# Performance work log

Hardware: AMD Instinct MI355X
Metric: run time of the kernel (lower is better)

The kernel has to match this reference:

```python
import jax, jax.numpy as jnp
import numpy as np

NOUN_VOCAB = 50000
FUNC_VOCAB = 10000
CTX_VOCAB = 50000
EMBED = 100
BATCH = 8192


def setup_inputs() -> dict:
    key = jax.random.key(0)
    k1, k2, k3, k4, k5, k6 = jax.random.split(key, 6)
    return {
        "X_argument": jax.random.randint(k1, (BATCH,), 0, NOUN_VOCAB, dtype=jnp.int32),
        "X_functor": jax.random.randint(k2, (BATCH,), 0, FUNC_VOCAB, dtype=jnp.int32),
        "X_context": jax.random.randint(k3, (BATCH,), 0, CTX_VOCAB, dtype=jnp.int32),
        # learned parameters
        "noun_matrix": jax.random.normal(k4, (NOUN_VOCAB, EMBED), dtype=jnp.float32),
        "functor_table": jax.random.normal(k5, (FUNC_VOCAB, EMBED * EMBED), dtype=jnp.float32),
        "context_table": jax.random.normal(k6, (CTX_VOCAB, EMBED), dtype=jnp.float32),
    }


def reference(X_argument, X_functor, X_context, noun_matrix, functor_table, context_table):
    arg_vecs = noun_matrix[X_argument]                       # [B, E]
    func_mats = functor_table[X_functor].reshape(-1, EMBED, EMBED)  # [B, E, E]
    ctx_vecs = context_table[X_context]                      # [B, E]
    # batched matvec (func matrix @ arg vector) then dot with context vector
    funcarg = jnp.einsum('bij,bj->bi', func_mats, arg_vecs)  # [B, E]
    return jnp.sum(funcarg * ctx_vecs, axis=1)               # [B]
```

## Files before the change

### kernel.cpp

```cpp
#include <hip/hip_runtime.h>

#define EMBED 100
#define MATSZ (EMBED * EMBED)
#define NVEC4 (MATSZ / 4)
#define BLOCK 256
#define ITERS 10

__global__ __launch_bounds__(BLOCK) void msg_kernel(
    const int* __restrict__ Xa,
    const int* __restrict__ Xf,
    const int* __restrict__ Xc,
    const float* __restrict__ noun_matrix,
    const float* __restrict__ functor_table,
    const float* __restrict__ context_table,
    float* __restrict__ out)
{
    const int b   = blockIdx.x;
    const int tid = threadIdx.x;

    __shared__ float4 s_arg4[EMBED / 4];
    __shared__ float  s_ctx[EMBED];
    __shared__ float  s_part[BLOCK / 64];

    const int ia  = Xa[b];
    const int ifn = Xf[b];
    const int ic  = Xc[b];

    if (tid < EMBED / 4) {
        s_arg4[tid] = ((const float4*)(noun_matrix + (size_t)ia * EMBED))[tid];
    }
    if (tid < EMBED) {
        s_ctx[tid] = context_table[(size_t)ic * EMBED + tid];
    }
    __syncthreads();

    const float4* __restrict__ M4 =
        (const float4*)(functor_table + (size_t)ifn * MATSZ);

    float4 mv[ITERS];
    #pragma unroll
    for (int k = 0; k < ITERS; ++k) {
        int v  = tid + k * BLOCK;
        int vc = v < NVEC4 ? v : (NVEC4 - 1);
        mv[k] = M4[vc];
    }

    float acc = 0.0f;
    #pragma unroll
    for (int k = 0; k < ITERS; ++k) {
        int v  = tid + k * BLOCK;
        int vc = v < NVEC4 ? v : (NVEC4 - 1);
        int f  = vc * 4;
        int i  = f / EMBED;
        int j  = f - i * EMBED;
        float4 a = s_arg4[j >> 2];
        float4 m = mv[k];
        float dot4 = m.x * a.x + m.y * a.y + m.z * a.z + m.w * a.w;
        float c = (v < NVEC4) ? s_ctx[i] : 0.0f;
        acc = fmaf(c, dot4, acc);
    }

    #pragma unroll
    for (int off = 32; off > 0; off >>= 1)
        acc += __shfl_down(acc, off, 64);

    const int wave = tid >> 6;
    const int lane = tid & 63;
    if (lane == 0) s_part[wave] = acc;
    __syncthreads();

    if (tid == 0) {
        float r = 0.0f;
        #pragma unroll
        for (int w = 0; w < BLOCK / 64; ++w) r += s_part[w];
        out[b] = r;
    }
}

extern "C" void kernel_launch(void* const* d_in, const int* in_sizes, int n_in,
                              void* d_out, int out_size, void* d_ws, size_t ws_size,
                              hipStream_t stream) {
    const int*   Xa   = (const int*)d_in[0];
    const int*   Xf   = (const int*)d_in[1];
    const int*   Xc   = (const int*)d_in[2];
    const float* noun = (const float*)d_in[3];
    const float* func = (const float*)d_in[4];
    const float* ctxt = (const float*)d_in[5];
    float*       out  = (float*)d_out;

    const int B = in_sizes[0];
    msg_kernel<<<B, BLOCK, 0, stream>>>(Xa, Xf, Xc, noun, func, ctxt, out);
}
```

Before: 509.6 us.

## Group batch rows by functor index to load each functor matrix once

Adds a workspace-based bucketing pass: a zero kernel and an atomic scatter kernel group batch indices by functor id (up to 8 per functor), plus a leftover list for any overflow. The main kernel then launches one block per functor vocabulary entry, loads that 40KB matrix once into registers and evaluates every batch row that uses it. This is meant to cut redundant reads of the functor table, since the 8192 rows draw from only 10000 functors and duplicates repeat the same matrix load. In exchange it adds three extra launches, atomics and per-row block syncs, and it launches 10000 blocks, most of which load nothing or exit early.

```diff
diff --git a/kernel.cpp b/kernel.cpp
--- a/kernel.cpp
+++ b/kernel.cpp
@@ -5,38 +5,58 @@
 #define NVEC4 (MATSZ / 4)
 #define BLOCK 256
 #define ITERS 10
+#define FUNC_VOCAB 10000
+#define K_CAP 8
+#define LEFT_BLOCKS 16
 
-__global__ __launch_bounds__(BLOCK) void msg_kernel(
+#define WS_COUNTS   0
+#define WS_LC       FUNC_VOCAB
+#define WS_BUCKET   10016
+#define WS_LEFT     (10016 + FUNC_VOCAB * K_CAP)
+
+__global__ __launch_bounds__(BLOCK) void zero_ws_kernel(int* __restrict__ w) {
+    int t = blockIdx.x * BLOCK + threadIdx.x;
+    if (t <= FUNC_VOCAB) w[t] = 0;
+}
+
+__global__ __launch_bounds__(BLOCK) void scatter_kernel(
+    const int* __restrict__ Xf, int* __restrict__ ws, int B)
+{
+    int t = blockIdx.x * BLOCK + threadIdx.x;
+    if (t >= B) return;
+    int f = Xf[t];
+    int slot = atomicAdd(&ws[WS_COUNTS + f], 1);
+    if (slot < K_CAP) {
+        ws[WS_BUCKET + f * K_CAP + slot] = t;
+    } else {
+        int s = atomicAdd(&ws[WS_LC], 1);
+        ws[WS_LEFT + s] = t;
+    }
+}
+
+__global__ __launch_bounds__(BLOCK) void pass2_kernel(
     const int* __restrict__ Xa,
-    const int* __restrict__ Xf,
     const int* __restrict__ Xc,
     const float* __restrict__ noun_matrix,
     const float* __restrict__ functor_table,
     const float* __restrict__ context_table,
-    float* __restrict__ out)
+    float* __restrict__ out,
+    const int* __restrict__ ws)
 {
-    const int b   = blockIdx.x;
+    const int f   = blockIdx.x;
     const int tid = threadIdx.x;
 
-    __shared__ float4 s_arg4[EMBED / 4];
-    __shared__ float  s_ctx[EMBED];
+    int c = ws[WS_COUNTS + f];
+    if (c <= 0) return;
+    if (c > K_CAP) c = K_CAP;
+
+    __shared__ float4 s_arg4[K_CAP][EMBED / 4];
+    __shared__ float  s_ctx [K_CAP][EMBED];
     __shared__ float  s_part[BLOCK / 64];
-
-    const int ia  = Xa[b];
-    const int ifn = Xf[b];
-    const int ic  = Xc[b];
-
-    if (tid < EMBED / 4) {
-        s_arg4[tid] = ((const float4*)(noun_matrix + (size_t)ia * EMBED))[tid];
-    }
-    if (tid < EMBED) {
-        s_ctx[tid] = context_table[(size_t)ic * EMBED + tid];
-    }
-    __syncthreads();
+    __shared__ int    s_b   [K_CAP];
 
     const float4* __restrict__ M4 =
-        (const float4*)(functor_table + (size_t)ifn * MATSZ);
-
+        (const float4*)(functor_table + (size_t)f * MATSZ);
     float4 mv[ITERS];
     #pragma unroll
     for (int k = 0; k < ITERS; ++k) {
@@ -45,35 +65,93 @@
         mv[k] = M4[vc];
     }
 
-    float acc = 0.0f;
-    #pragma unroll
-    for (int k = 0; k < ITERS; ++k) {
-        int v  = tid + k * BLOCK;
-        int vc = v < NVEC4 ? v : (NVEC4 - 1);
-        int f  = vc * 4;
-        int i  = f / EMBED;
-        int j  = f - i * EMBED;
-        float4 a = s_arg4[j >> 2];
-        float4 m = mv[k];
-        float dot4 = m.x * a.x + m.y * a.y + m.z * a.z + m.w * a.w;
-        float c = (v < NVEC4) ? s_ctx[i] : 0.0f;
-        acc = fmaf(c, dot4, acc);
+    const int p = tid >> 5;
+    const int r = tid & 31;
+    if (p < c) {
+        int b = ws[WS_BUCKET + f * K_CAP + p];
+        if (r == 0) s_b[p] = b;
+        if (r < EMBED / 4) {
+            s_arg4[p][r] = ((const float4*)(noun_matrix  + (size_t)Xa[b] * EMBED))[r];
+            ((float4*)s_ctx[p])[r] = ((const float4*)(context_table + (size_t)Xc[b] * EMBED))[r];
+        }
     }
-
-    #pragma unroll
-    for (int off = 32; off > 0; off >>= 1)
-        acc += __shfl_down(acc, off, 64);
-
-    const int wave = tid >> 6;
-    const int lane = tid & 63;
-    if (lane == 0) s_part[wave] = acc;
     __syncthreads();
 
-    if (tid == 0) {
-        float r = 0.0f;
+    for (int p2 = 0; p2 < c; ++p2) {
+        float acc = 0.0f;
         #pragma unroll
-        for (int w = 0; w < BLOCK / 64; ++w) r += s_part[w];
-        out[b] = r;
+        for (int k = 0; k < ITERS; ++k) {
+            int v  = tid + k * BLOCK;
+            int vc = v < NVEC4 ? v : (NVEC4 - 1);
+            int fi = vc * 4;
+            int i  = fi / EMBED;
+            int j  = fi - i * EMBED;
+            float4 a = s_arg4[p2][j >> 2];
+            float4 m = mv[k];
+            float d4 = m.x * a.x + m.y * a.y + m.z * a.z + m.w * a.w;
+            float cc = (v < NVEC4) ? s_ctx[p2][i] : 0.0f;
+            acc = fmaf(cc, d4, acc);
+        }
+        #pragma unroll
+        for (int off = 32; off > 0; off >>= 1)
+            acc += __shfl_down(acc, off, 64);
+        if ((tid & 63) == 0) s_part[tid >> 6] = acc;
+        __syncthreads();
+        if (tid == 0)
+            out[s_b[p2]] = s_part[0] + s_part[1] + s_part[2] + s_part[3];
+        __syncthreads();
+    }
+}
+
+__global__ __launch_bounds__(BLOCK) void leftover_kernel(
+    const int* __restrict__ Xa,
+    const int* __restrict__ Xf,
+    const int* __restrict__ Xc,
+    const float* __restrict__ noun_matrix,
+    const float* __restrict__ functor_table,
+    const float* __restrict__ context_table,
+    float* __restrict__ out,
+    const int* __restrict__ ws)
+{
+    const int tid = threadIdx.x;
+    const int n   = ws[WS_LC];
+
+    __shared__ float4 s_arg4[EMBED / 4];
+    __shared__ float  s_ctx[EMBED];
+    __shared__ float  s_part[BLOCK / 64];
+
+    for (int idx = blockIdx.x; idx < n; idx += LEFT_BLOCKS) {
+        int b = ws[WS_LEFT + idx];
+        if (tid < EMBED / 4) {
+            s_arg4[tid] = ((const float4*)(noun_matrix + (size_t)Xa[b] * EMBED))[tid];
+            ((float4*)s_ctx)[tid] = ((const float4*)(context_table + (size_t)Xc[b] * EMBED))[tid];
+        }
+        __syncthreads();
+
+        const float4* __restrict__ M4 =
+            (const float4*)(functor_table + (size_t)Xf[b] * MATSZ);
+        float acc = 0.0f;
+        #pragma unroll
+        for (int k = 0; k < ITERS; ++k) {
+            int v  = tid + k * BLOCK;
+            int vc = v < NVEC4 ? v : (NVEC4 - 1);
+            int fi = vc * 4;
+            int i  = fi / EMBED;
+            int j  = fi - i * EMBED;
+            float4 a = s_arg4[j >> 2];
+            float4 m = M4[vc];
+            float d4 = m.x * a.x + m.y * a.y + m.z * a.z + m.w * a.w;
+            float cc = (v < NVEC4) ? s_ctx[i] : 0.0f;
+            acc = fmaf(cc, d4, acc);
+        }
+        #pragma unroll
+        for (int off = 32; off > 0; off >>= 1)
+            acc += __shfl_down(acc, off, 64);
+        if ((tid & 63) == 0) s_part[tid >> 6] = acc;
+        __syncthreads();
+        if (tid == 0)
+            out[b] = s_part[0] + s_part[1] + s_part[2] + s_part[3];
+        __syncthreads();
     }
 }
 
@@ -87,7 +165,12 @@
     const float* func = (const float*)d_in[4];
     const float* ctxt = (const float*)d_in[5];
     float*       out  = (float*)d_out;
+    int*         ws   = (int*)d_ws;
 
     const int B = in_sizes[0];
-    msg_kernel<<<B, BLOCK, 0, stream>>>(Xa, Xf, Xc, noun, func, ctxt, out);
+
+    zero_ws_kernel<<<(FUNC_VOCAB + BLOCK) / BLOCK, BLOCK, 0, stream>>>(ws);
+    scatter_kernel<<<(B + BLOCK - 1) / BLOCK, BLOCK, 0, stream>>>(Xf, ws, B);
+    pass2_kernel<<<FUNC_VOCAB, BLOCK, 0, stream>>>(Xa, Xc, noun, func, ctxt, out, ws);
+    leftover_kernel<<<LEFT_BLOCKS, BLOCK, 0, stream>>>(Xa, Xf, Xc, noun, func, ctxt, out, ws);
 }
```

Result: no change. 513.7 us (+0.8%).
